# Performance work log

Measured on AMD Instinct MI355X. Metric: run time of the kernel, lower is better.

## Reference

```python
import jax, jax.numpy as jnp
import numpy as np

N = 50000      # nodes
E = 800000     # edges (before self loops)
IN = 128       # in_channels == hidden*heads so residuals fire
HID = 32       # hidden_channels
H = 4          # num_heads
OUT = 64       # out_channels
EPS = 1e-5
SLOPE = 0.2    # GATv2 leaky_relu negative slope


def setup_inputs() -> dict:
    key = jax.random.key(0)
    ks = jax.random.split(key, 32)
    s = 0.05
    d = {
        'x': jax.random.normal(ks[0], (N, IN), jnp.float32),
        'edge_index': jax.random.randint(ks[1], (2, E), 0, N, jnp.int64),
        'bn_in_gamma': jnp.ones((IN,), jnp.float32),
        'bn_in_beta': jnp.zeros((IN,), jnp.float32),
        # conv0: IN -> H*HID
        'conv0_Wl': jax.random.normal(ks[2], (IN, H * HID), jnp.float32) * s,
        'conv0_bl': jnp.zeros((H * HID,), jnp.float32),
        'conv0_Wr': jax.random.normal(ks[3], (IN, H * HID), jnp.float32) * s,
        'conv0_br': jnp.zeros((H * HID,), jnp.float32),
        'conv0_att': jax.random.normal(ks[4], (H, HID), jnp.float32) * s,
        'conv0_bias': jnp.zeros((H * HID,), jnp.float32),
        'bn0_gamma': jnp.ones((H * HID,), jnp.float32),
        'bn0_beta': jnp.zeros((H * HID,), jnp.float32),
        # conv1: H*HID -> H*HID
        'conv1_Wl': jax.random.normal(ks[5], (H * HID, H * HID), jnp.float32) * s,
        'conv1_bl': jnp.zeros((H * HID,), jnp.float32),
        'conv1_Wr': jax.random.normal(ks[6], (H * HID, H * HID), jnp.float32) * s,
        'conv1_br': jnp.zeros((H * HID,), jnp.float32),
        'conv1_att': jax.random.normal(ks[7], (H, HID), jnp.float32) * s,
        'conv1_bias': jnp.zeros((H * HID,), jnp.float32),
        'bn1_gamma': jnp.ones((H * HID,), jnp.float32),
        'bn1_beta': jnp.zeros((H * HID,), jnp.float32),
        # conv2: H*HID -> OUT, heads=1, concat=False
        'conv2_Wl': jax.random.normal(ks[8], (H * HID, OUT), jnp.float32) * s,
        'conv2_bl': jnp.zeros((OUT,), jnp.float32),
        'conv2_Wr': jax.random.normal(ks[9], (H * HID, OUT), jnp.float32) * s,
        'conv2_br': jnp.zeros((OUT,), jnp.float32),
        'conv2_att': jax.random.normal(ks[10], (1, OUT), jnp.float32) * s,
        'conv2_bias': jnp.zeros((OUT,), jnp.float32),
        # classifier: Linear(OUT, HID) -> ReLU -> Linear(HID, OUT)
        'cls_w1': jax.random.normal(ks[11], (OUT, HID), jnp.float32) * s,
        'cls_b1': jnp.zeros((HID,), jnp.float32),
        'cls_w2': jax.random.normal(ks[12], (HID, OUT), jnp.float32) * s,
        'cls_b2': jnp.zeros((OUT,), jnp.float32),
    }
    return d


def _bn(x, gamma, beta):
    m = x.mean(0)
    v = x.var(0)
    return gamma * (x - m) * jax.lax.rsqrt(v + EPS) + beta


def _gatv2(x, src, dst, Wl, bl, Wr, br, att, bias, concat):
    # GATv2Conv (share_weights=False): e_ij = att . leaky_relu(xl[j] + xr[i])
    h, c = att.shape
    n = x.shape[0]
    xl = (x @ Wl + bl).reshape(n, h, c)   # source transform
    xr = (x @ Wr + br).reshape(n, h, c)   # target transform
    e = jax.nn.leaky_relu(xl[src] + xr[dst], SLOPE)       # [Etot, H, C]
    score = jnp.einsum('ehc,hc->eh', e, att)              # [Etot, H]
    smax = jax.ops.segment_max(score, dst, num_segments=n)
    p = jnp.exp(score - smax[dst])
    denom = jax.ops.segment_sum(p, dst, num_segments=n)
    alpha = p / denom[dst]                                # segment softmax over dst
    msg = xl[src] * alpha[:, :, None]                     # [Etot, H, C]
    out = jax.ops.segment_sum(msg, dst, num_segments=n)   # [N, H, C]
    out = out.reshape(n, h * c) if concat else out.mean(axis=1)
    return out + bias


def reference(x, edge_index, bn_in_gamma, bn_in_beta,
              conv0_Wl, conv0_bl, conv0_Wr, conv0_br, conv0_att, conv0_bias,
              bn0_gamma, bn0_beta,
              conv1_Wl, conv1_bl, conv1_Wr, conv1_br, conv1_att, conv1_bias,
              bn1_gamma, bn1_beta,
              conv2_Wl, conv2_bl, conv2_Wr, conv2_br, conv2_att, conv2_bias,
              cls_w1, cls_b1, cls_w2, cls_b2):
    n = x.shape[0]
    loop = jnp.arange(n, dtype=edge_index.dtype)
    src = jnp.concatenate([edge_index[0], loop])  # add_self_loops=True
    dst = jnp.concatenate([edge_index[1], loop])

    h = _bn(x, bn_in_gamma, bn_in_beta)

    # layer 0 (residual fires: IN == H*HID)
    res = h
    h = _gatv2(h, src, dst, conv0_Wl, conv0_bl, conv0_Wr, conv0_br, conv0_att, conv0_bias, True)
    h = jax.nn.elu(_bn(h, bn0_gamma, bn0_beta))
    h = h + res

    # layer 1
    res = h
    h = _gatv2(h, src, dst, conv1_Wl, conv1_bl, conv1_Wr, conv1_br, conv1_att, conv1_bias, True)
    h = jax.nn.elu(_bn(h, bn1_gamma, bn1_beta))
    h = h + res

    # final conv: heads=1, concat=False
    h = _gatv2(h, src, dst, conv2_Wl, conv2_bl, conv2_Wr, conv2_br, conv2_att, conv2_bias, False)

    # classifier MLP (dropout is identity in eval)
    h = jax.nn.relu(h @ cls_w1 + cls_b1)
    return h @ cls_w2 + cls_b2
```

## Files before the change

### kernel.cpp

```cpp
#include <hip/hip_runtime.h>
#include <math.h>

typedef __attribute__((ext_vector_type(8))) short short8;
typedef __attribute__((ext_vector_type(4))) float f32x4;

constexpr float EPS_BN = 1e-5f;
constexpr float SLOPE = 0.2f;

__device__ __forceinline__ unsigned short f2bf_rne(float f) {
    unsigned u = __float_as_uint(f);
    unsigned r = ((u >> 16) & 1u) + 0x7fffu;
    return (unsigned short)((u + r) >> 16);
}
__device__ __forceinline__ float bf2f(unsigned short h) {
    return __uint_as_float(((unsigned)h) << 16);
}

__global__ void col_stats_kernel(const float* __restrict__ data,
                                 float* __restrict__ stats, int n, int c) {
    int f = threadIdx.x;
    float s = 0.0f, q = 0.0f;
    for (int r = blockIdx.x; r < n; r += gridDim.x) {
        float v = data[(size_t)r * c + f];
        s += v;
        q += v * v;
    }
    atomicAdd(&stats[f], s);
    atomicAdd(&stats[c + f], q);
}

__global__ void bn_apply_kernel(const float4* __restrict__ x, const float* __restrict__ stats,
                                const float* __restrict__ g, const float* __restrict__ b,
                                float4* __restrict__ h, int n, int c) {
    int c4 = c / 4;
    int i = blockIdx.x * blockDim.x + threadIdx.x;
    if (i >= n * c4) return;
    int f = (i % c4) * 4;
    float4 v = x[i];
    float4 o;
    float invn = 1.0f / (float)n;
#pragma unroll
    for (int j = 0; j < 4; j++) {
        float mean = stats[f + j] * invn;
        float var = stats[c + f + j] * invn - mean * mean;
        float rs = rsqrtf(var + EPS_BN);
        float xv = (&v.x)[j];
        (&o.x)[j] = g[f + j] * (xv - mean) * rs + b[f + j];
    }
    h[i] = o;
}

__global__ void bn_elu_res_kernel(const float4* __restrict__ out, const float* __restrict__ stats,
                                  const float* __restrict__ g, const float* __restrict__ b,
                                  const float4* __restrict__ res, float4* __restrict__ dst,
                                  int n, int c) {
    int c4 = c / 4;
    int i = blockIdx.x * blockDim.x + threadIdx.x;
    if (i >= n * c4) return;
    int f = (i % c4) * 4;
    float4 v = out[i];
    float4 r = res[i];
    float4 o;
    float invn = 1.0f / (float)n;
#pragma unroll
    for (int j = 0; j < 4; j++) {
        float mean = stats[f + j] * invn;
        float var = stats[c + f + j] * invn - mean * mean;
        float rs = rsqrtf(var + EPS_BN);
        float y = g[f + j] * ((&v.x)[j] - mean) * rs + b[f + j];
        float e = (y > 0.0f) ? y : expm1f(y);
        (&o.x)[j] = e + (&r.x)[j];
    }
    dst[i] = o;
}

__global__ __launch_bounds__(256) void gemm_mfma_kernel(
        const float* __restrict__ X, const float* __restrict__ W,
        const float* __restrict__ bias, float* __restrict__ Y, int n, int m) {
    __shared__ short sA[2][2][4][64][8];
    __shared__ short sB[2][2][4][64][8];
    int t = threadIdx.x;
    int col0 = blockIdx.x * 64;
    int row0 = blockIdx.y * 64;
    int wid = t >> 6, lane = t & 63;
    int wr = wid >> 1, wc = wid & 1;

    f32x4 acc[2][2];
#pragma unroll
    for (int i = 0; i < 2; i++)
#pragma unroll
        for (int j = 0; j < 2; j++) acc[i][j] = (f32x4){0.f, 0.f, 0.f, 0.f};

    for (int half = 0; half < 2; half++) {
#pragma unroll
        for (int s0 = 0; s0 < 2; s0++) {
            int s = t + s0 * 256;
            int l = s & 63, rb = (s >> 6) & 3, ks2 = s >> 8;
            int row = row0 + rb * 16 + (l & 15);
            int kb = (half * 2 + ks2) * 32 + (l >> 4) * 8;
            short8 hv = {}; short8 lv = {};
            if (row < n) {
                const float4* p = (const float4*)&X[(size_t)row * 128 + kb];
                float4 v0 = p[0], v1 = p[1];
#pragma unroll
                for (int j = 0; j < 4; j++) {
                    float f0 = (&v0.x)[j];
                    unsigned short h0 = f2bf_rne(f0);
                    hv[j] = (short)h0;
                    lv[j] = (short)f2bf_rne(f0 - bf2f(h0));
                    float f1 = (&v1.x)[j];
                    unsigned short h1 = f2bf_rne(f1);
                    hv[4 + j] = (short)h1;
                    lv[4 + j] = (short)f2bf_rne(f1 - bf2f(h1));
                }
            }
            *(short8*)&sA[0][ks2][rb][l][0] = hv;
            *(short8*)&sA[1][ks2][rb][l][0] = lv;
        }
#pragma unroll
        for (int s0 = 0; s0 < 2; s0++) {
            int s = t + s0 * 256;
            int l = s & 63, nb = (s >> 6) & 3, ks2 = s >> 8;
            int col = col0 + nb * 16 + (l & 15);
            int kb = (half * 2 + ks2) * 32 + (l >> 4) * 8;
            short8 hv, lv;
#pragma unroll
            for (int j = 0; j < 8; j++) {
                float f = W[(size_t)(kb + j) * m + col];
                unsigned short h = f2bf_rne(f);
                hv[j] = (short)h;
                lv[j] = (short)f2bf_rne(f - bf2f(h));
            }
            *(short8*)&sB[0][ks2][nb][l][0] = hv;
            *(short8*)&sB[1][ks2][nb][l][0] = lv;
        }
        __syncthreads();
#pragma unroll
        for (int ks2 = 0; ks2 < 2; ks2++) {
            short8 Ah[2], Al[2], Bh[2], Bl[2];
#pragma unroll
            for (int mr = 0; mr < 2; mr++) {
                Ah[mr] = *(const short8*)&sA[0][ks2][wr * 2 + mr][lane][0];
                Al[mr] = *(const short8*)&sA[1][ks2][wr * 2 + mr][lane][0];
            }
#pragma unroll
            for (int nr = 0; nr < 2; nr++) {
                Bh[nr] = *(const short8*)&sB[0][ks2][wc * 2 + nr][lane][0];
                Bl[nr] = *(const short8*)&sB[1][ks2][wc * 2 + nr][lane][0];
            }
#pragma unroll
            for (int mr = 0; mr < 2; mr++)
#pragma unroll
                for (int nr = 0; nr < 2; nr++) {
                    acc[mr][nr] = __builtin_amdgcn_mfma_f32_16x16x32_bf16(Ah[mr], Bh[nr], acc[mr][nr], 0, 0, 0);
                    acc[mr][nr] = __builtin_amdgcn_mfma_f32_16x16x32_bf16(Ah[mr], Bl[nr], acc[mr][nr], 0, 0, 0);
                    acc[mr][nr] = __builtin_amdgcn_mfma_f32_16x16x32_bf16(Al[mr], Bh[nr], acc[mr][nr], 0, 0, 0);
                }
        }
        __syncthreads();
    }
    int cbase = col0 + wc * 32 + (lane & 15);
#pragma unroll
    for (int mr = 0; mr < 2; mr++)
#pragma unroll
        for (int nr = 0; nr < 2; nr++) {
            int col = cbase + nr * 16;
            float bv = bias[col];
#pragma unroll
            for (int r = 0; r < 4; r++) {
                int row = row0 + wr * 32 + mr * 16 + (lane >> 4) * 4 + r;
                if (row < n) Y[(size_t)row * m + col] = acc[mr][nr][r] + bv;
            }
        }
}

__global__ void degree_kernel(const int* __restrict__ ei, int E, int Et, int* __restrict__ deg) {
    int e = blockIdx.x * blockDim.x + threadIdx.x;
    if (e >= Et) return;
    int dst = (e < E) ? ei[E + e] : e - E;
    atomicAdd(&deg[dst], 1);
}

__global__ void blocksum_kernel(const int* __restrict__ deg, int n, int* __restrict__ bsum) {
    __shared__ int sd[256];
    int i = blockIdx.x * 256 + threadIdx.x;
    sd[threadIdx.x] = (i < n) ? deg[i] : 0;
    __syncthreads();
    for (int s = 128; s > 0; s >>= 1) {
        if (threadIdx.x < s) sd[threadIdx.x] += sd[threadIdx.x + s];
        __syncthreads();
    }
    if (threadIdx.x == 0) bsum[blockIdx.x] = sd[0];
}

__global__ void scanb_kernel(int* __restrict__ bsum, int nb) {
    __shared__ int sd[256];
    int tid = threadIdx.x;
    int v = (tid < nb) ? bsum[tid] : 0;
    sd[tid] = v;
    __syncthreads();
    for (int off = 1; off < 256; off <<= 1) {
        int t = (tid >= off) ? sd[tid - off] : 0;
        __syncthreads();
        sd[tid] += t;
        __syncthreads();
    }
    if (tid < nb) bsum[tid] = sd[tid] - v;
}

__global__ void rowptr_kernel(const int* __restrict__ deg, const int* __restrict__ bofs,
                              int n, int* __restrict__ rowptr, int* __restrict__ cursor) {
    __shared__ int sd[256];
    int tid = threadIdx.x;
    int i = blockIdx.x * 256 + tid;
    int v = (i < n) ? deg[i] : 0;
    sd[tid] = v;
    __syncthreads();
    for (int off = 1; off < 256; off <<= 1) {
        int t = (tid >= off) ? sd[tid - off] : 0;
        __syncthreads();
        sd[tid] += t;
        __syncthreads();
    }
    int excl = bofs[blockIdx.x] + sd[tid] - v;
    if (i < n) { rowptr[i] = excl; cursor[i] = excl; }
    if (i == n - 1) rowptr[n] = excl + v;
}

__global__ void scatter_kernel(const int* __restrict__ ei, int E, int Et,
                               int* __restrict__ cursor, int* __restrict__ srcs) {
    int e = blockIdx.x * blockDim.x + threadIdx.x;
    if (e >= Et) return;
    int src, dst;
    if (e < E) { src = ei[e]; dst = ei[E + e]; }
    else       { src = dst = e - E; }
    int pos = atomicAdd(&cursor[dst], 1);
    srcs[pos] = src;
}

template <int H, int C, int VPL>
__global__ __launch_bounds__(256) void gat_gather_kernel(
        const float* __restrict__ xl, const float* __restrict__ xr,
        const float* __restrict__ att, const float* __restrict__ bias,
        const int* __restrict__ rowptr, const int* __restrict__ srcs,
        float* __restrict__ out, int n) {
    int wid = (blockIdx.x * 256 + threadIdx.x) >> 6;
    int lane = threadIdx.x & 63;
    if (wid >= n) return;
    constexpr int HC = H * C;
    constexpr int LPH = C / VPL;
    int base = lane * VPL;

    float xrv[VPL], av[VPL];
#pragma unroll
    for (int v = 0; v < VPL; v++) {
        xrv[v] = xr[(size_t)wid * HC + base + v];
        av[v] = att[base + v];
    }
    float m = 0.0f, denom = 0.0f;
    float acc[VPL];
#pragma unroll
    for (int v = 0; v < VPL; v++) acc[v] = 0.0f;

    int beg = rowptr[wid], end = rowptr[wid + 1];
    for (int chunk = beg; chunk < end; chunk += 64) {
        int cn = min(64, end - chunk);
        int my_src = (chunk + lane < end) ? srcs[chunk + lane] : 0;
        int src = __shfl(my_src, 0, 64);
        float xlv[VPL];
        if (VPL == 2) {
            float2 tv = *(const float2*)&xl[(size_t)src * HC + base];
            xlv[0] = tv.x; xlv[1] = tv.y;
        } else {
            xlv[0] = xl[(size_t)src * HC + base];
        }
        for (int j = 0; j < cn; j++) {
            float nxt[VPL];
            int nj = (j + 1 < cn) ? j + 1 : j;
            int nsrc = __shfl(my_src, nj, 64);
            if (VPL == 2) {
                float2 tv = *(const float2*)&xl[(size_t)nsrc * HC + base];
                nxt[0] = tv.x; nxt[1] = tv.y;
            } else {
                nxt[0] = xl[(size_t)nsrc * HC + base];
            }
            float s = 0.0f;
#pragma unroll
            for (int v = 0; v < VPL; v++) {
                float u = xlv[v] + xrv[v];
                u = (u >= 0.0f) ? u : SLOPE * u;
                s += u * av[v];
            }
#pragma unroll
            for (int off = 1; off < LPH; off <<= 1) s += __shfl_xor(s, off, 64);
            if (s > m + 8.0f) {
                float sc = __expf(m - s);
                denom *= sc;
#pragma unroll
                for (int v = 0; v < VPL; v++) acc[v] *= sc;
                m = s;
            }
            float p = __expf(s - m);
            denom += p;
#pragma unroll
            for (int v = 0; v < VPL; v++) acc[v] = fmaf(p, xlv[v], acc[v]);
#pragma unroll
            for (int v = 0; v < VPL; v++) xlv[v] = nxt[v];
        }
    }
    float inv = 1.0f / denom;
    if (VPL == 2) {
        float2 o = make_float2(acc[0] * inv + bias[base], acc[1] * inv + bias[base + 1]);
        *(float2*)&out[(size_t)wid * HC + base] = o;
    } else {
        out[(size_t)wid * HC + base] = acc[0] * inv + bias[base];
    }
}

__global__ __launch_bounds__(256) void classifier_kernel(
        const float* __restrict__ out2,
        const float* __restrict__ W1, const float* __restrict__ b1,
        const float* __restrict__ W2, const float* __restrict__ b2,
        float* __restrict__ y, int n) {
    __shared__ float sW1[64 * 32];
    __shared__ float sW2[32 * 64];
    __shared__ float sb1[32], sb2[64];
    int t = threadIdx.x;
    for (int i = t; i < 2048; i += 256) { sW1[i] = W1[i]; sW2[i] = W2[i]; }
    if (t < 32) sb1[t] = b1[t];
    if (t < 64) sb2[t] = b2[t];
    __syncthreads();
    int node = blockIdx.x * blockDim.x + t;
    if (node >= n) return;
    float v[64];
    const float4* src4 = (const float4*)&out2[(size_t)node * 64];
#pragma unroll
    for (int i = 0; i < 16; i++) {
        float4 f = src4[i];
        v[4 * i + 0] = f.x; v[4 * i + 1] = f.y; v[4 * i + 2] = f.z; v[4 * i + 3] = f.w;
    }
    float hid[32];
#pragma unroll
    for (int j = 0; j < 32; j++) {
        float s = sb1[j];
#pragma unroll
        for (int i = 0; i < 64; i++) s += v[i] * sW1[i * 32 + j];
        hid[j] = fmaxf(s, 0.0f);
    }
    float4* y4 = (float4*)&y[(size_t)node * 64];
#pragma unroll
    for (int o4 = 0; o4 < 16; o4++) {
        float4 o;
#pragma unroll
        for (int j = 0; j < 4; j++) {
            int o_ = o4 * 4 + j;
            float s = sb2[o_];
#pragma unroll
            for (int k = 0; k < 32; k++) s += hid[k] * sW2[k * 64 + o_];
            (&o.x)[j] = s;
        }
        y4[o4] = o;
    }
}

extern "C" void kernel_launch(void* const* d_in, const int* in_sizes, int n_in,
                              void* d_out, int out_size, void* d_ws, size_t ws_size,
                              hipStream_t stream) {
    const float* x        = (const float*)d_in[0];
    const int*   ei       = (const int*)d_in[1];
    const float* bn_in_g  = (const float*)d_in[2];
    const float* bn_in_b  = (const float*)d_in[3];
    const float* c0_Wl    = (const float*)d_in[4];
    const float* c0_bl    = (const float*)d_in[5];
    const float* c0_Wr    = (const float*)d_in[6];
    const float* c0_br    = (const float*)d_in[7];
    const float* c0_att   = (const float*)d_in[8];
    const float* c0_bias  = (const float*)d_in[9];
    const float* bn0_g    = (const float*)d_in[10];
    const float* bn0_b    = (const float*)d_in[11];
    const float* c1_Wl    = (const float*)d_in[12];
    const float* c1_bl    = (const float*)d_in[13];
    const float* c1_Wr    = (const float*)d_in[14];
    const float* c1_br    = (const float*)d_in[15];
    const float* c1_att   = (const float*)d_in[16];
    const float* c1_bias  = (const float*)d_in[17];
    const float* bn1_g    = (const float*)d_in[18];
    const float* bn1_b    = (const float*)d_in[19];
    const float* c2_Wl    = (const float*)d_in[20];
    const float* c2_bl    = (const float*)d_in[21];
    const float* c2_Wr    = (const float*)d_in[22];
    const float* c2_br    = (const float*)d_in[23];
    const float* c2_att   = (const float*)d_in[24];
    const float* c2_bias  = (const float*)d_in[25];
    const float* cls_w1   = (const float*)d_in[26];
    const float* cls_b1   = (const float*)d_in[27];
    const float* cls_w2   = (const float*)d_in[28];
    const float* cls_b2   = (const float*)d_in[29];

    const int N = in_sizes[0] / 128;
    const int E = in_sizes[1] / 2;
    const int Et = E + N;

    float* ws = (float*)d_ws;
    size_t off = 0;
    auto alloc = [&](size_t nf) { float* p = ws + off; off += nf; return p; };
    float* hA     = alloc((size_t)N * 128);
    float* xlb    = alloc((size_t)N * 128);
    float* xrb    = alloc((size_t)N * 128);
    float* outb   = alloc((size_t)N * 128);
    float* stats  = alloc(256);
    int* deg      = (int*)alloc(N);
    int* rowptr   = (int*)alloc(N + 1);
    int* cursor   = (int*)alloc(N);
    int* srcs     = (int*)alloc(Et);
    int* bsum     = (int*)alloc(256);

    const int et_blocks = (Et + 255) / 256;
    const int elem128   = (N * 32 + 255) / 256;
    const int nb        = (N + 255) / 256;
    const int gw        = (N + 3) / 4;
    dim3 gemm_grid_128(2, (N + 63) / 64);
    dim3 gemm_grid_64(1, (N + 63) / 64);

    hipMemsetAsync(deg, 0, (size_t)N * sizeof(int), stream);
    degree_kernel<<<et_blocks, 256, 0, stream>>>(ei, E, Et, deg);
    blocksum_kernel<<<nb, 256, 0, stream>>>(deg, N, bsum);
    scanb_kernel<<<1, 256, 0, stream>>>(bsum, nb);
    rowptr_kernel<<<nb, 256, 0, stream>>>(deg, bsum, N, rowptr, cursor);
    scatter_kernel<<<et_blocks, 256, 0, stream>>>(ei, E, Et, cursor, srcs);

    hipMemsetAsync(stats, 0, 256 * sizeof(float), stream);
    col_stats_kernel<<<512, 128, 0, stream>>>(x, stats, N, 128);
    bn_apply_kernel<<<elem128, 256, 0, stream>>>((const float4*)x, stats, bn_in_g, bn_in_b,
                                                 (float4*)hA, N, 128);

    float* h = hA;

    gemm_mfma_kernel<<<gemm_grid_128, 256, 0, stream>>>(h, c0_Wl, c0_bl, xlb, N, 128);
    gemm_mfma_kernel<<<gemm_grid_128, 256, 0, stream>>>(h, c0_Wr, c0_br, xrb, N, 128);
    gat_gather_kernel<4, 32, 2><<<gw, 256, 0, stream>>>(xlb, xrb, c0_att, c0_bias, rowptr, srcs, outb, N);
    hipMemsetAsync(stats, 0, 256 * sizeof(float), stream);
    col_stats_kernel<<<512, 128, 0, stream>>>(outb, stats, N, 128);
    bn_elu_res_kernel<<<elem128, 256, 0, stream>>>((const float4*)outb, stats, bn0_g, bn0_b,
                                                   (const float4*)h, (float4*)xrb, N, 128);
    h = xrb;

    gemm_mfma_kernel<<<gemm_grid_128, 256, 0, stream>>>(h, c1_Wl, c1_bl, xlb, N, 128);
    gemm_mfma_kernel<<<gemm_grid_128, 256, 0, stream>>>(h, c1_Wr, c1_br, hA, N, 128);
    gat_gather_kernel<4, 32, 2><<<gw, 256, 0, stream>>>(xlb, hA, c1_att, c1_bias, rowptr, srcs, outb, N);
    hipMemsetAsync(stats, 0, 256 * sizeof(float), stream);
    col_stats_kernel<<<512, 128, 0, stream>>>(outb, stats, N, 128);
    bn_elu_res_kernel<<<elem128, 256, 0, stream>>>((const float4*)outb, stats, bn1_g, bn1_b,
                                                   (const float4*)h, (float4*)hA, N, 128);
    h = hA;

    gemm_mfma_kernel<<<gemm_grid_64, 256, 0, stream>>>(h, c2_Wl, c2_bl, xlb, N, 64);
    gemm_mfma_kernel<<<gemm_grid_64, 256, 0, stream>>>(h, c2_Wr, c2_br, xrb, N, 64);
    gat_gather_kernel<1, 64, 1><<<gw, 256, 0, stream>>>(xlb, xrb, c2_att, c2_bias, rowptr, srcs, outb, N);

    classifier_kernel<<<(N + 255) / 256, 256, 0, stream>>>(outb, cls_w1, cls_b1,
                                                           cls_w2, cls_b2, (float*)d_out, N);
}
```

Measured before the change: 733.5 us.

## Process four edges per wavefront step in GAT gather with online-softmax merge

The gather kernel now splits each 64-lane wavefront into four 16-lane groups. Each group handles a different neighbor edge per iteration and loads float4 vectors. The partial online-softmax states (max, denom, acc) are then merged across groups with shuffles before one group writes the output. This cuts the serial per-edge loop length by four and widens memory requests per lane. Separately, the per-layer stats memsets are replaced by one enlarged memset covering three stats buffers placed after deg, which removes two memset launches but relies on those buffers sitting contiguously right after deg.

```diff
diff --git a/kernel.cpp b/kernel.cpp
--- a/kernel.cpp
+++ b/kernel.cpp
@@ -238,61 +238,71 @@
     srcs[pos] = src;
 }
 
-template <int H, int C, int VPL>
+template <int H, int C>
 __global__ __launch_bounds__(256) void gat_gather_kernel(
         const float* __restrict__ xl, const float* __restrict__ xr,
         const float* __restrict__ att, const float* __restrict__ bias,
         const int* __restrict__ rowptr, const int* __restrict__ srcs,
         float* __restrict__ out, int n) {
+    constexpr int HC = H * C;
+    constexpr int VPL = HC / 16;
+    constexpr int RPH = C / VPL;
     int wid = (blockIdx.x * 256 + threadIdx.x) >> 6;
     int lane = threadIdx.x & 63;
     if (wid >= n) return;
-    constexpr int HC = H * C;
-    constexpr int LPH = C / VPL;
-    int base = lane * VPL;
-
-    float xrv[VPL], av[VPL];
+    int g = lane >> 4, wl = lane & 15;
+    int base = wl * VPL;
+
+    float xrv[VPL], av[VPL], acc[VPL];
 #pragma unroll
     for (int v = 0; v < VPL; v++) {
         xrv[v] = xr[(size_t)wid * HC + base + v];
         av[v] = att[base + v];
+        acc[v] = 0.0f;
     }
     float m = 0.0f, denom = 0.0f;
-    float acc[VPL];
-#pragma unroll
-    for (int v = 0; v < VPL; v++) acc[v] = 0.0f;
 
     int beg = rowptr[wid], end = rowptr[wid + 1];
     for (int chunk = beg; chunk < end; chunk += 64) {
         int cn = min(64, end - chunk);
         int my_src = (chunk + lane < end) ? srcs[chunk + lane] : 0;
-        int src = __shfl(my_src, 0, 64);
+        int iters = (cn + 3) >> 2;
+        int slot = g;
+        bool val = slot < cn;
+        int src = __shfl(my_src, slot, 64);
         float xlv[VPL];
-        if (VPL == 2) {
-            float2 tv = *(const float2*)&xl[(size_t)src * HC + base];
-            xlv[0] = tv.x; xlv[1] = tv.y;
-        } else {
-            xlv[0] = xl[(size_t)src * HC + base];
-        }
-        for (int j = 0; j < cn; j++) {
+        {
+            const float4* p = (const float4*)&xl[(size_t)src * HC + base];
+            float4 a = p[0];
+            xlv[0] = a.x; xlv[1] = a.y; xlv[2] = a.z; xlv[3] = a.w;
+            if (VPL == 8) {
+                float4 b_ = p[1];
+                xlv[4] = b_.x; xlv[5] = b_.y; xlv[6] = b_.z; xlv[7] = b_.w;
+            }
+        }
+        for (int j = 0; j < iters; j++) {
+            int nslot = slot + 4;
+            int nsrc = __shfl(my_src, nslot & 63, 64);
             float nxt[VPL];
-            int nj = (j + 1 < cn) ? j + 1 : j;
-            int nsrc = __shfl(my_src, nj, 64);
-            if (VPL == 2) {
-                float2 tv = *(const float2*)&xl[(size_t)nsrc * HC + base];
-                nxt[0] = tv.x; nxt[1] = tv.y;
-            } else {
-                nxt[0] = xl[(size_t)nsrc * HC + base];
+            {
+                const float4* p = (const float4*)&xl[(size_t)nsrc * HC + base];
+                float4 a = p[0];
+                nxt[0] = a.x; nxt[1] = a.y; nxt[2] = a.z; nxt[3] = a.w;
+                if (VPL == 8) {
+                    float4 b_ = p[1];
+                    nxt[4] = b_.x; nxt[5] = b_.y; nxt[6] = b_.z; nxt[7] = b_.w;
+                }
             }
             float s = 0.0f;
 #pragma unroll
             for (int v = 0; v < VPL; v++) {
                 float u = xlv[v] + xrv[v];
                 u = (u >= 0.0f) ? u : SLOPE * u;
-                s += u * av[v];
-            }
-#pragma unroll
-            for (int off = 1; off < LPH; off <<= 1) s += __shfl_xor(s, off, 64);
+                s = fmaf(u, av[v], s);
+            }
+#pragma unroll
+            for (int off = 1; off < RPH; off <<= 1) s += __shfl_xor(s, off, 64);
+            if (!val) s = -1.0e30f;
             if (s > m + 8.0f) {
                 float sc = __expf(m - s);
                 denom *= sc;
@@ -306,14 +316,42 @@
             for (int v = 0; v < VPL; v++) acc[v] = fmaf(p, xlv[v], acc[v]);
 #pragma unroll
             for (int v = 0; v < VPL; v++) xlv[v] = nxt[v];
-        }
-    }
-    float inv = 1.0f / denom;
-    if (VPL == 2) {
-        float2 o = make_float2(acc[0] * inv + bias[base], acc[1] * inv + bias[base + 1]);
-        *(float2*)&out[(size_t)wid * HC + base] = o;
-    } else {
-        out[(size_t)wid * HC + base] = acc[0] * inv + bias[base];
+            val = nslot < cn;
+            slot = nslot;
+        }
+    }
+#pragma unroll
+    for (int step = 16; step <= 32; step <<= 1) {
+        float om = __shfl_xor(m, step, 64);
+        float od = __shfl_xor(denom, step, 64);
+        float oa[VPL];
+#pragma unroll
+        for (int v = 0; v < VPL; v++) oa[v] = __shfl_xor(acc[v], step, 64);
+        float mn = fmaxf(m, om);
+        float sa = __expf(m - mn);
+        float sb = __expf(om - mn);
+        denom = denom * sa + od * sb;
+#pragma unroll
+        for (int v = 0; v < VPL; v++) acc[v] = acc[v] * sa + oa[v] * sb;
+        m = mn;
+    }
+    if (g == 0) {
+        float inv = 1.0f / denom;
+        float4 o0;
+        o0.x = acc[0] * inv + bias[base + 0];
+        o0.y = acc[1] * inv + bias[base + 1];
+        o0.z = acc[2] * inv + bias[base + 2];
+        o0.w = acc[3] * inv + bias[base + 3];
+        float4* po = (float4*)&out[(size_t)wid * HC + base];
+        po[0] = o0;
+        if (VPL == 8) {
+            float4 o1;
+            o1.x = acc[4] * inv + bias[base + 4];
+            o1.y = acc[5] * inv + bias[base + 5];
+            o1.z = acc[6] * inv + bias[base + 6];
+            o1.w = acc[7] * inv + bias[base + 7];
+            po[1] = o1;
+        }
     }
 }
 
@@ -408,8 +446,10 @@
     float* xlb    = alloc((size_t)N * 128);
     float* xrb    = alloc((size_t)N * 128);
     float* outb   = alloc((size_t)N * 128);
-    float* stats  = alloc(256);
     int* deg      = (int*)alloc(N);
+    float* statsI = alloc(256);
+    float* stats0 = alloc(256);
+    float* stats1 = alloc(256);
     int* rowptr   = (int*)alloc(N + 1);
     int* cursor   = (int*)alloc(N);
     int* srcs     = (int*)alloc(Et);
@@ -422,41 +462,39 @@
     dim3 gemm_grid_128(2, (N + 63) / 64);
     dim3 gemm_grid_64(1, (N + 63) / 64);
 
-    hipMemsetAsync(deg, 0, (size_t)N * sizeof(int), stream);
+    hipMemsetAsync(deg, 0, ((size_t)N + 768) * sizeof(int), stream);
+
     degree_kernel<<<et_blocks, 256, 0, stream>>>(ei, E, Et, deg);
     blocksum_kernel<<<nb, 256, 0, stream>>>(deg, N, bsum);
     scanb_kernel<<<1, 256, 0, stream>>>(bsum, nb);
     rowptr_kernel<<<nb, 256, 0, stream>>>(deg, bsum, N, rowptr, cursor);
     scatter_kernel<<<et_blocks, 256, 0, stream>>>(ei, E, Et, cursor, srcs);
 
-    hipMemsetAsync(stats, 0, 256 * sizeof(float), stream);
-    col_stats_kernel<<<512, 128, 0, stream>>>(x, stats, N, 128);
-    bn_apply_kernel<<<elem128, 256, 0, stream>>>((const float4*)x, stats, bn_in_g, bn_in_b,
+    col_stats_kernel<<<512, 128, 0, stream>>>(x, statsI, N, 128);
+    bn_apply_kernel<<<elem128, 256, 0, stream>>>((const float4*)x, statsI, bn_in_g, bn_in_b,
                                                  (float4*)hA, N, 128);
 
     float* h = hA;
 
     gemm_mfma_kernel<<<gemm_grid_128, 256, 0, stream>>>(h, c0_Wl, c0_bl, xlb, N, 128);
     gemm_mfma_kernel<<<gemm_grid_128, 256, 0, stream>>>(h, c0_Wr, c0_br, xrb, N, 128);
-    gat_gather_kernel<4, 32, 2><<<gw, 256, 0, stream>>>(xlb, xrb, c0_att, c0_bias, rowptr, srcs, outb, N);
-    hipMemsetAsync(stats, 0, 256 * sizeof(float), stream);
-    col_stats_kernel<<<512, 128, 0, stream>>>(outb, stats, N, 128);
-    bn_elu_res_kernel<<<elem128, 256, 0, stream>>>((const float4*)outb, stats, bn0_g, bn0_b,
+    gat_gather_kernel<4, 32><<<gw, 256, 0, stream>>>(xlb, xrb, c0_att, c0_bias, rowptr, srcs, outb, N);
+    col_stats_kernel<<<512, 128, 0, stream>>>(outb, stats0, N, 128);
+    bn_elu_res_kernel<<<elem128, 256, 0, stream>>>((const float4*)outb, stats0, bn0_g, bn0_b,
                                                    (const float4*)h, (float4*)xrb, N, 128);
     h = xrb;
 
     gemm_mfma_kernel<<<gemm_grid_128, 256, 0, stream>>>(h, c1_Wl, c1_bl, xlb, N, 128);
     gemm_mfma_kernel<<<gemm_grid_128, 256, 0, stream>>>(h, c1_Wr, c1_br, hA, N, 128);
-    gat_gather_kernel<4, 32, 2><<<gw, 256, 0, stream>>>(xlb, hA, c1_att, c1_bias, rowptr, srcs, outb, N);
-    hipMemsetAsync(stats, 0, 256 * sizeof(float), stream);
-    col_stats_kernel<<<512, 128, 0, stream>>>(outb, stats, N, 128);
-    bn_elu_res_kernel<<<elem128, 256, 0, stream>>>((const float4*)outb, stats, bn1_g, bn1_b,
+    gat_gather_kernel<4, 32><<<gw, 256, 0, stream>>>(xlb, hA, c1_att, c1_bias, rowptr, srcs, outb, N);
+    col_stats_kernel<<<512, 128, 0, stream>>>(outb, stats1, N, 128);
+    bn_elu_res_kernel<<<elem128, 256, 0, stream>>>((const float4*)outb, stats1, bn1_g, bn1_b,
                                                    (const float4*)h, (float4*)hA, N, 128);
     h = hA;
 
     gemm_mfma_kernel<<<gemm_grid_64, 256, 0, stream>>>(h, c2_Wl, c2_bl, xlb, N, 64);
     gemm_mfma_kernel<<<gemm_grid_64, 256, 0, stream>>>(h, c2_Wr, c2_br, xrb, N, 64);
-    gat_gather_kernel<1, 64, 1><<<gw, 256, 0, stream>>>(xlb, xrb, c2_att, c2_bias, rowptr, srcs, outb, N);
+    gat_gather_kernel<1, 64><<<gw, 256, 0, stream>>>(xlb, xrb, c2_att, c2_bias, rowptr, srcs, outb, N);
 
     classifier_kernel<<<(N + 255) / 256, 256, 0, stream>>>(outb, cls_w1, cls_b1,
                                                            cls_w2, cls_b2, (float*)d_out, N);
```

Result: faster. 677.4 us (-7.6%).
